# Optimization experiments

Hardware: AMD Instinct MI355X
Metric: run time of the kernel (lower is better)

## Reference

```python
import jax, jax.numpy as jnp
import numpy as np

B, T, E, H = 16, 1024, 1024, 16
DH = E // H  # 64, divisible by 4
THETA = 10000.0


def setup_inputs() -> dict:
    key = jax.random.key(0)
    ks = jax.random.split(key, 10)
    inp = {
        "hidden_states": jax.random.normal(ks[0], (B, T, E), dtype=jnp.float32),
        "rope_pos": jax.random.randint(ks[1], (B, T, 2), 0, 32, dtype=jnp.int32),
    }
    s = 0.02
    inp["Wq"] = jax.random.normal(ks[2], (E, E), dtype=jnp.float32) * s
    inp["bq"] = jnp.zeros((E,), dtype=jnp.float32)
    inp["Wk"] = jax.random.normal(ks[3], (E, E), dtype=jnp.float32) * s
    inp["bk"] = jnp.zeros((E,), dtype=jnp.float32)
    inp["Wv"] = jax.random.normal(ks[4], (E, E), dtype=jnp.float32) * s
    inp["bv"] = jnp.zeros((E,), dtype=jnp.float32)
    inp["Wo"] = jax.random.normal(ks[5], (E, E), dtype=jnp.float32) * s
    inp["bo"] = jnp.zeros((E,), dtype=jnp.float32)
    return inp


def _rotate_half(x):
    # interleaved pairs: (x0,x1,x2,x3,...) -> (-x1,x0,-x3,x2,...)
    x_even = x[..., ::2]
    x_odd = x[..., 1::2]
    return jnp.stack((-x_odd, x_even), axis=-1).reshape(x.shape)


def _apply_rope_2d(q, k, rope_pos, theta):
    Dh = q.shape[-1]
    half, quarter = Dh // 2, Dh // 4
    dtype = q.dtype
    idx = jnp.arange(quarter, dtype=dtype)
    inv = (theta ** (-2.0 * idx / quarter)).astype(dtype)  # [quarter]
    pos_h = rope_pos[..., 0].astype(dtype)[..., None]  # [B,T,1]
    pos_w = rope_pos[..., 1].astype(dtype)[..., None]
    ang_h = pos_h * inv  # [B,T,quarter]
    ang_w = pos_w * inv
    ri = lambda a: jnp.repeat(a, 2, axis=-1)[:, None]  # -> [B,1,T,half]
    cos_h, sin_h = ri(jnp.cos(ang_h)), ri(jnp.sin(ang_h))
    cos_w, sin_w = ri(jnp.cos(ang_w)), ri(jnp.sin(ang_w))
    q_h, q_w = q[..., :half], q[..., half:]
    k_h, k_w = k[..., :half], k[..., half:]
    q_h = q_h * cos_h + _rotate_half(q_h) * sin_h
    k_h = k_h * cos_h + _rotate_half(k_h) * sin_h
    q_w = q_w * cos_w + _rotate_half(q_w) * sin_w
    k_w = k_w * cos_w + _rotate_half(k_w) * sin_w
    return jnp.concatenate([q_h, q_w], axis=-1), jnp.concatenate([k_h, k_w], axis=-1)


def reference(hidden_states, rope_pos, Wq, bq, Wk, bk, Wv, bv, Wo, bo):
    b, t, e = hidden_states.shape
    scale = DH ** -0.5
    # torch nn.Linear: y = x @ W.T + b, W is [out, in]
    proj = lambda x, W, bias: jnp.einsum('bte,oe->bto', x, W) + bias
    q = proj(hidden_states, Wq, bq).reshape(b, t, H, DH).transpose(0, 2, 1, 3)
    k = proj(hidden_states, Wk, bk).reshape(b, t, H, DH).transpose(0, 2, 1, 3)
    v = proj(hidden_states, Wv, bv).reshape(b, t, H, DH).transpose(0, 2, 1, 3)
    q, k = _apply_rope_2d(q, k, rope_pos, THETA)
    # eager attention: scores in input dtype, softmax in float32
    scores = jnp.einsum('bhqd,bhkd->bhqk', q, k) * scale
    w = jax.nn.softmax(scores.astype(jnp.float32), axis=-1).astype(q.dtype)
    out = jnp.einsum('bhqk,bhkd->bhqd', w, v)
    out = out.transpose(0, 2, 1, 3).reshape(b, t, e)
    return jnp.einsum('bte,oe->bto', out, Wo) + bo
```

## Files before the change

### kernel.cpp

```cpp
#include <hip/hip_runtime.h>
#include <hip/hip_bf16.h>

#define B_  16
#define T_  1024
#define E_  1024
#define H_  16
#define DH_ 64

typedef short s16x8 __attribute__((ext_vector_type(8)));
typedef float f32x4 __attribute__((ext_vector_type(4)));
typedef unsigned short u16x4 __attribute__((ext_vector_type(4)));

__device__ __forceinline__ void async_cp16(const void* g, void* l) {
  __builtin_amdgcn_global_load_lds(
      (__attribute__((address_space(1))) unsigned int*)(g),
      (__attribute__((address_space(3))) unsigned int*)(l), 16, 0, 0);
}

__device__ __forceinline__ s16x8 frag8(const void* p) { return *(const s16x8*)p; }

__device__ __forceinline__ float fexp2(float x) {
#if __has_builtin(__builtin_amdgcn_exp2f)
  return __builtin_amdgcn_exp2f(x);
#else
  return exp2f(x);
#endif
}

__device__ __forceinline__ unsigned short f2bu(float x) {
  __hip_bfloat16 h = __float2bfloat16(x);
  return *reinterpret_cast<unsigned short*>(&h);
}

__global__ __launch_bounds__(256) void cast_f32_bf16(const float* __restrict__ in,
                                                     __hip_bfloat16* __restrict__ out,
                                                     int n4) {
  int i = blockIdx.x * 256 + threadIdx.x;
  if (i >= n4) return;
  float4 v = ((const float4*)in)[i];
  __hip_bfloat16* o = out + (size_t)i * 4;
  o[0] = __float2bfloat16(v.x);
  o[1] = __float2bfloat16(v.y);
  o[2] = __float2bfloat16(v.z);
  o[3] = __float2bfloat16(v.w);
}

#define GEMM_CORE(A_, B_PTR_, K_)                                              \
  __shared__ __align__(16) __hip_bfloat16 As[128 * 64];                        \
  __shared__ __align__(16) __hip_bfloat16 Bs[128 * 64];                        \
  const int tid  = threadIdx.x;                                                \
  const int lane = tid & 63, wave = tid >> 6;                                  \
  const int col  = lane & 15, quad = lane >> 4;                                \
  const int wm = (wave >> 1) << 6, wn = (wave & 1) << 6;                       \
  const f32x4 fzero = {0.f, 0.f, 0.f, 0.f};                                    \
  f32x4 acc[4][4];                                                             \
  _Pragma("unroll") for (int i = 0; i < 4; i++)                                \
    _Pragma("unroll") for (int j = 0; j < 4; j++) acc[i][j] = fzero;           \
  const int r8 = lane >> 3;                                                    \
  const int kgs = (lane & 7) ^ (r8 & 7);                                       \
  const char* Asrc[4]; const char* Bsrc[4]; char* Adst[4]; char* Bdst[4];      \
  _Pragma("unroll") for (int u = 0; u < 4; u++) {                              \
    int ch = u * 4 + wave;                                                     \
    int row = ch * 8 + r8;                                                     \
    Asrc[u] = (const char*)(A_ + (size_t)(bm + row) * K_) + kgs * 16;          \
    Bsrc[u] = (const char*)(B_PTR_ + (size_t)(bn + row) * K_) + kgs * 16;      \
    Adst[u] = (char*)As + ch * 1024;                                           \
    Bdst[u] = (char*)Bs + ch * 1024;                                           \
  }                                                                            \
  const int sw0 = ((quad) ^ (col & 7)) * 16;                                   \
  const int sw1 = ((quad + 4) ^ (col & 7)) * 16;                               \
  for (int kt = 0; kt < (K_ >> 6); ++kt) {                                     \
    __syncthreads();                                                           \
    const int koff = kt * 128;                                                 \
    _Pragma("unroll") for (int u = 0; u < 4; u++) {                            \
      async_cp16(Asrc[u] + koff, Adst[u]);                                     \
      async_cp16(Bsrc[u] + koff, Bdst[u]);                                     \
    }                                                                          \
    __syncthreads();                                                           \
    s16x8 af[2][4], bf[2][4];                                                  \
    _Pragma("unroll") for (int i = 0; i < 4; i++) {                            \
      af[0][i] = frag8((const char*)As + (wm + i * 16 + col) * 128 + sw0);     \
      af[1][i] = frag8((const char*)As + (wm + i * 16 + col) * 128 + sw1);     \
    }                                                                          \
    _Pragma("unroll") for (int j = 0; j < 4; j++) {                            \
      bf[0][j] = frag8((const char*)Bs + (wn + j * 16 + col) * 128 + sw0);     \
      bf[1][j] = frag8((const char*)Bs + (wn + j * 16 + col) * 128 + sw1);     \
    }                                                                          \
    _Pragma("unroll") for (int i = 0; i < 4; i++)                              \
      _Pragma("unroll") for (int j = 0; j < 4; j++) {                          \
        acc[i][j] = __builtin_amdgcn_mfma_f32_16x16x32_bf16(af[0][i], bf[0][j], acc[i][j], 0, 0, 0); \
        acc[i][j] = __builtin_amdgcn_mfma_f32_16x16x32_bf16(af[1][i], bf[1][j], acc[i][j], 0, 0, 0); \
      }                                                                        \
  }

__global__ __launch_bounds__(256, 2) void gemm_qkv(const __hip_bfloat16* __restrict__ A,
                                                   const __hip_bfloat16* __restrict__ Wqkv,
                                                   const float* __restrict__ bq,
                                                   const float* __restrict__ bk,
                                                   const float* __restrict__ bv,
                                                   __hip_bfloat16* __restrict__ Qb,
                                                   __hip_bfloat16* __restrict__ Kb,
                                                   __hip_bfloat16* __restrict__ Vt) {
  const int bm = (blockIdx.x & 127) << 7;
  const int bn = (blockIdx.x >> 7) << 7;
  GEMM_CORE(A, Wqkv, 1024)

  const int seg = bn >> 10;
  const float* bp = (seg == 0) ? bq : (seg == 1) ? bk : bv;
  float bcol[4];
#pragma unroll
  for (int j = 0; j < 4; j++) bcol[j] = bp[(bn & 1023) + wn + j * 16 + col];
#pragma unroll
  for (int i = 0; i < 4; i++) {
#pragma unroll
    for (int j = 0; j < 4; j++) {
      const int nc = (bn & 1023) + wn + j * 16 + col;
#pragma unroll
      for (int r = 0; r < 4; r++) {
        const int grow = bm + wm + i * 16 + quad * 4 + r;
        float v = acc[i][j][r] + bcol[j];
        if (seg == 0) {
          Qb[(size_t)grow * 1024 + nc] = __float2bfloat16(v);
        } else if (seg == 1) {
          Kb[(size_t)grow * 1024 + nc] = __float2bfloat16(v);
        } else {
          int bb = grow >> 10, tt = grow & 1023;
          int hh = nc >> 6, dd = nc & 63;
          Vt[(((size_t)bb * H_ + hh) * DH_ + dd) * T_ + tt] = __float2bfloat16(v);
        }
      }
    }
  }
}

__global__ __launch_bounds__(256, 2) void gemm_out(const __hip_bfloat16* __restrict__ A,
                                                   const __hip_bfloat16* __restrict__ Bw,
                                                   const float* __restrict__ bias,
                                                   float* __restrict__ Cout) {
  const int bm = (blockIdx.x & 127) << 7;
  const int bn = (blockIdx.x >> 7) << 7;
  GEMM_CORE(A, Bw, 1024)

  float bcol[4];
#pragma unroll
  for (int j = 0; j < 4; j++) bcol[j] = bias[bn + wn + j * 16 + col];
#pragma unroll
  for (int i = 0; i < 4; i++)
#pragma unroll
    for (int j = 0; j < 4; j++) {
      const int gcol = bn + wn + j * 16 + col;
#pragma unroll
      for (int r = 0; r < 4; r++) {
        const int grow = bm + wm + i * 16 + quad * 4 + r;
        Cout[(size_t)grow * 1024 + gcol] = acc[i][j][r] + bcol[j];
      }
    }
}

__global__ __launch_bounds__(256) void rope2d(__hip_bfloat16* __restrict__ Q,
                                              __hip_bfloat16* __restrict__ K,
                                              const int* __restrict__ pos) {
  const int row = blockIdx.x;
  const int t   = threadIdx.x;
  const float ph = (float)pos[row * 2 + 0];
  const float pw = (float)pos[row * 2 + 1];
  const int pd = (2 * t) & 31;
  float cs[2], sn[2];
#pragma unroll
  for (int i = 0; i < 2; i++) {
    int pdi = pd + i;
    int f = pdi & 15;
    float p = (pdi & 16) ? pw : ph;
    float inv = __expf((float)f * (-1.1512925464970229f));
    float ang = p * inv;
    cs[i] = cosf(ang);
    sn[i] = sinf(ang);
  }
  const float QSC = 0.18033688011112043f;
  size_t base = (size_t)row * E_ + 4 * t;
  {
    __hip_bfloat16* P = Q;
    float e0 = __bfloat162float(P[base + 0]);
    float e1 = __bfloat162float(P[base + 1]);
    float e2 = __bfloat162float(P[base + 2]);
    float e3 = __bfloat162float(P[base + 3]);
    P[base + 0] = __float2bfloat16((e0 * cs[0] - e1 * sn[0]) * QSC);
    P[base + 1] = __float2bfloat16((e1 * cs[0] + e0 * sn[0]) * QSC);
    P[base + 2] = __float2bfloat16((e2 * cs[1] - e3 * sn[1]) * QSC);
    P[base + 3] = __float2bfloat16((e3 * cs[1] + e2 * sn[1]) * QSC);
  }
  {
    __hip_bfloat16* P = K;
    float e0 = __bfloat162float(P[base + 0]);
    float e1 = __bfloat162float(P[base + 1]);
    float e2 = __bfloat162float(P[base + 2]);
    float e3 = __bfloat162float(P[base + 3]);
    P[base + 0] = __float2bfloat16(e0 * cs[0] - e1 * sn[0]);
    P[base + 1] = __float2bfloat16(e1 * cs[0] + e0 * sn[0]);
    P[base + 2] = __float2bfloat16(e2 * cs[1] - e3 * sn[1]);
    P[base + 3] = __float2bfloat16(e3 * cs[1] + e2 * sn[1]);
  }
}

__global__ __launch_bounds__(256, 3) void attn_flash(const __hip_bfloat16* __restrict__ Q,
                                                     const __hip_bfloat16* __restrict__ Kt,
                                                     const __hip_bfloat16* __restrict__ Vt,
                                                     __hip_bfloat16* __restrict__ Oa) {
  __shared__ __align__(16) __hip_bfloat16 QP[128 * 72];
  __shared__ __align__(16) __hip_bfloat16 Ks[64 * 72];
  __shared__ __align__(16) __hip_bfloat16 Vs[64 * 72];

  const int bid = blockIdx.x;
  const int bh = bid >> 3;
  const int b = bh >> 4, h = bh & 15;
  const int qt = bid & 7;
  const int tid = threadIdx.x;
  const int lane = tid & 63, wave = tid >> 6;
  const int col = lane & 15, quad = lane >> 4;

  const size_t qrow0 = (size_t)b * T_ + qt * 128;

#pragma unroll
  for (int cc = 0; cc < 4; ++cc) {
    int c = tid + cc * 256;
    int r = c >> 3, k8 = c & 7;
    const float4* src = (const float4*)((const char*)(Q + (qrow0 + r) * E_ + h * DH_)) + k8;
    *(float4*)((char*)QP + r * 144 + k8 * 16) = *src;
  }

  const f32x4 fzero = {0.f, 0.f, 0.f, 0.f};
  f32x4 o[2][4];
  float lr[2] = {0.f, 0.f};
#pragma unroll
  for (int g = 0; g < 2; g++)
#pragma unroll
    for (int j = 0; j < 4; j++) o[g][j] = fzero;
  s16x8 qf[2][2];
  char* Pw = (char*)QP + wave * 32 * 144;

  for (int kt2 = 0; kt2 < 16; ++kt2) {
    __syncthreads();
    const int kb = kt2 * 64;
#pragma unroll
    for (int cc = 0; cc < 4; ++cc) {
      int c = tid + cc * 256;
      if (c < 512) {
        int r = c >> 3, k8 = c & 7;
        const float4* src = (const float4*)((const char*)(Kt + ((size_t)b * T_ + kb + r) * E_ + h * DH_)) + k8;
        *(float4*)((char*)Ks + r * 144 + k8 * 16) = *src;
      } else {
        int c2 = c - 512;
        int d = c2 >> 3, k8 = c2 & 7;
        const float4* src = (const float4*)((const char*)(Vt + (((size_t)b * H_ + h) * DH_ + d) * T_ + kb)) + k8;
        *(float4*)((char*)Vs + d * 144 + k8 * 16) = *src;
      }
    }
    __syncthreads();
    if (kt2 == 0) {
#pragma unroll
      for (int g = 0; g < 2; g++) {
        qf[g][0] = frag8((const char*)QP + (g * 64 + wave * 16 + col) * 144 + quad * 16);
        qf[g][1] = frag8((const char*)QP + (g * 64 + wave * 16 + col) * 144 + 64 + quad * 16);
      }
      __syncthreads();
    }
    s16x8 kf[4][2];
#pragma unroll
    for (int ktile = 0; ktile < 4; ktile++) {
      kf[ktile][0] = frag8((const char*)Ks + (ktile * 16 + col) * 144 + quad * 16);
      kf[ktile][1] = frag8((const char*)Ks + (ktile * 16 + col) * 144 + 64 + quad * 16);
    }
#pragma unroll
    for (int g = 0; g < 2; g++) {
#pragma unroll
      for (int ktile = 0; ktile < 4; ktile++) {
        f32x4 d = fzero;
        d = __builtin_amdgcn_mfma_f32_16x16x32_bf16(kf[ktile][0], qf[g][0], d, 0, 0, 0);
        d = __builtin_amdgcn_mfma_f32_16x16x32_bf16(kf[ktile][1], qf[g][1], d, 0, 0, 0);
        float p0 = fexp2(d[0]), p1 = fexp2(d[1]), p2 = fexp2(d[2]), p3 = fexp2(d[3]);
        lr[g] += (p0 + p1) + (p2 + p3);
        u16x4 pk = {f2bu(p0), f2bu(p1), f2bu(p2), f2bu(p3)};
        *(u16x4*)(Pw + (g * 16 + col) * 144 + ktile * 32 + quad * 8) = pk;
      }
    }
    s16x8 vf[4][2];
#pragma unroll
    for (int jm = 0; jm < 4; jm++) {
      vf[jm][0] = frag8((const char*)Vs + (jm * 16 + col) * 144 + quad * 16);
      vf[jm][1] = frag8((const char*)Vs + (jm * 16 + col) * 144 + 64 + quad * 16);
    }
#pragma unroll
    for (int g = 0; g < 2; g++) {
      s16x8 pf0 = frag8(Pw + (g * 16 + col) * 144 + quad * 16);
      s16x8 pf1 = frag8(Pw + (g * 16 + col) * 144 + 64 + quad * 16);
#pragma unroll
      for (int jm = 0; jm < 4; jm++) {
        o[g][jm] = __builtin_amdgcn_mfma_f32_16x16x32_bf16(vf[jm][0], pf0, o[g][jm], 0, 0, 0);
        o[g][jm] = __builtin_amdgcn_mfma_f32_16x16x32_bf16(vf[jm][1], pf1, o[g][jm], 0, 0, 0);
      }
    }
  }
#pragma unroll
  for (int g = 0; g < 2; g++) {
    lr[g] += __shfl_xor(lr[g], 16, 64);
    lr[g] += __shfl_xor(lr[g], 32, 64);
  }
#pragma unroll
  for (int g = 0; g < 2; g++) {
    float invl = 1.f / lr[g];
    size_t grow = qrow0 + g * 64 + wave * 16 + col;
    char* obase = (char*)(Oa + grow * E_ + h * DH_);
#pragma unroll
    for (int jm = 0; jm < 4; jm++) {
      u16x4 pk = {f2bu(o[g][jm][0] * invl), f2bu(o[g][jm][1] * invl),
                  f2bu(o[g][jm][2] * invl), f2bu(o[g][jm][3] * invl)};
      *(u16x4*)(obase + jm * 32 + quad * 8) = pk;
    }
  }
}

extern "C" void kernel_launch(void* const* d_in, const int* in_sizes, int n_in,
                              void* d_out, int out_size, void* d_ws, size_t ws_size,
                              hipStream_t stream) {
  const float* X   = (const float*)d_in[0];
  const int*   pos = (const int*)d_in[1];
  const float* Wq  = (const float*)d_in[2];
  const float* bq  = (const float*)d_in[3];
  const float* Wk  = (const float*)d_in[4];
  const float* bk  = (const float*)d_in[5];
  const float* Wv  = (const float*)d_in[6];
  const float* bv  = (const float*)d_in[7];
  const float* Wo  = (const float*)d_in[8];
  const float* bo  = (const float*)d_in[9];
  float* out = (float*)d_out;

  char* ws = (char*)d_ws;
  const size_t MB = 1024 * 1024;
  __hip_bfloat16* Xb    = (__hip_bfloat16*)(ws + 0 * MB);
  __hip_bfloat16* Qb    = (__hip_bfloat16*)(ws + 32 * MB);
  __hip_bfloat16* Kb    = (__hip_bfloat16*)(ws + 64 * MB);
  __hip_bfloat16* Vtb   = (__hip_bfloat16*)(ws + 96 * MB);
  __hip_bfloat16* Wqkvb = (__hip_bfloat16*)(ws + 128 * MB);
  __hip_bfloat16* Wob   = (__hip_bfloat16*)(ws + 136 * MB);
  __hip_bfloat16* Ab    = Xb;

  cast_f32_bf16<<<16384, 256, 0, stream>>>(X,  Xb,  4194304);
  cast_f32_bf16<<<1024,  256, 0, stream>>>(Wq, Wqkvb,           262144);
  cast_f32_bf16<<<1024,  256, 0, stream>>>(Wk, Wqkvb + 1048576, 262144);
  cast_f32_bf16<<<1024,  256, 0, stream>>>(Wv, Wqkvb + 2097152, 262144);
  cast_f32_bf16<<<1024,  256, 0, stream>>>(Wo, Wob,             262144);

  gemm_qkv<<<3072, 256, 0, stream>>>(Xb, Wqkvb, bq, bk, bv, Qb, Kb, Vtb);

  rope2d<<<16384, 256, 0, stream>>>(Qb, Kb, pos);
  attn_flash<<<2048, 256, 0, stream>>>(Qb, Kb, Vtb, Ab);

  gemm_out<<<1024, 256, 0, stream>>>(Ab, Wob, bo, out);
}
```

Baseline: 445.0 us.

## Fuse 2D RoPE into QKV GEMM epilogue and batch weight casts

Moves the 2D rotary embedding and Q scaling into the QKV GEMM epilogue, using a lane shuffle to fetch each pair partner and the hardware sin/cos builtins on angles reduced to revolutions. This removes the separate rope2d kernel, which re-read and re-wrote Q and K in global memory. It also merges the four weight-cast launches into one kernel and raises the attention kernel's occupancy hint from 3 to 4 waves. The risks are extra register pressure and transcendental work in the GEMM epilogue, plus small accuracy differences from the fast sin/cos approximation.

```diff
diff --git a/kernel.cpp b/kernel.cpp
--- a/kernel.cpp
+++ b/kernel.cpp
@@ -27,6 +27,21 @@
 #endif
 }
 
+__device__ __forceinline__ float fsin2pi(float rev) {
+#if __has_builtin(__builtin_amdgcn_sinf)
+  return __builtin_amdgcn_sinf(rev);
+#else
+  return sinf(rev * 6.283185307179586f);
+#endif
+}
+__device__ __forceinline__ float fcos2pi(float rev) {
+#if __has_builtin(__builtin_amdgcn_cosf)
+  return __builtin_amdgcn_cosf(rev);
+#else
+  return cosf(rev * 6.283185307179586f);
+#endif
+}
+
 __device__ __forceinline__ unsigned short f2bu(float x) {
   __hip_bfloat16 h = __float2bfloat16(x);
   return *reinterpret_cast<unsigned short*>(&h);
@@ -37,6 +52,22 @@
                                                      int n4) {
   int i = blockIdx.x * 256 + threadIdx.x;
   if (i >= n4) return;
+  float4 v = ((const float4*)in)[i];
+  __hip_bfloat16* o = out + (size_t)i * 4;
+  o[0] = __float2bfloat16(v.x);
+  o[1] = __float2bfloat16(v.y);
+  o[2] = __float2bfloat16(v.z);
+  o[3] = __float2bfloat16(v.w);
+}
+
+__global__ __launch_bounds__(256) void cast_w4(const float* __restrict__ w0, const float* __restrict__ w1,
+                                               const float* __restrict__ w2, const float* __restrict__ w3,
+                                               __hip_bfloat16* __restrict__ o0, __hip_bfloat16* __restrict__ o1,
+                                               __hip_bfloat16* __restrict__ o2, __hip_bfloat16* __restrict__ o3) {
+  int seg = blockIdx.x >> 10;
+  const float* in = (seg == 0) ? w0 : (seg == 1) ? w1 : (seg == 2) ? w2 : w3;
+  __hip_bfloat16* out = (seg == 0) ? o0 : (seg == 1) ? o1 : (seg == 2) ? o2 : o3;
+  int i = (blockIdx.x & 1023) * 256 + threadIdx.x;
   float4 v = ((const float4*)in)[i];
   __hip_bfloat16* o = out + (size_t)i * 4;
   o[0] = __float2bfloat16(v.x);
@@ -98,6 +129,7 @@
                                                    const float* __restrict__ bq,
                                                    const float* __restrict__ bk,
                                                    const float* __restrict__ bv,
+                                                   const int* __restrict__ pos,
                                                    __hip_bfloat16* __restrict__ Qb,
                                                    __hip_bfloat16* __restrict__ Kb,
                                                    __hip_bfloat16* __restrict__ Vt) {
@@ -110,24 +142,58 @@
   float bcol[4];
 #pragma unroll
   for (int j = 0; j < 4; j++) bcol[j] = bp[(bn & 1023) + wn + j * 16 + col];
-#pragma unroll
-  for (int i = 0; i < 4; i++) {
-#pragma unroll
-    for (int j = 0; j < 4; j++) {
-      const int nc = (bn & 1023) + wn + j * 16 + col;
-#pragma unroll
-      for (int r = 0; r < 4; r++) {
-        const int grow = bm + wm + i * 16 + quad * 4 + r;
-        float v = acc[i][j][r] + bcol[j];
-        if (seg == 0) {
-          Qb[(size_t)grow * 1024 + nc] = __float2bfloat16(v);
-        } else if (seg == 1) {
-          Kb[(size_t)grow * 1024 + nc] = __float2bfloat16(v);
-        } else {
+
+  if (seg == 2) {
+#pragma unroll
+    for (int i = 0; i < 4; i++)
+#pragma unroll
+      for (int j = 0; j < 4; j++) {
+        const int nc = (bn & 1023) + wn + j * 16 + col;
+#pragma unroll
+        for (int r = 0; r < 4; r++) {
+          const int grow = bm + wm + i * 16 + quad * 4 + r;
+          float v = acc[i][j][r] + bcol[j];
           int bb = grow >> 10, tt = grow & 1023;
           int hh = nc >> 6, dd = nc & 63;
           Vt[(((size_t)bb * H_ + hh) * DH_ + dd) * T_ + tt] = __float2bfloat16(v);
         }
+      }
+    return;
+  }
+
+  const float NL2T = -1.6609640474436811f;
+  const float inv0 = fexp2(NL2T * (float)(col >> 1));
+  const float inv1 = fexp2(NL2T * (float)(8 + (col >> 1)));
+  const float sgn  = (col & 1) ? 1.f : -1.f;
+  const float R2PI = 0.15915494309189535f;
+  const float QSC  = 0.18033688011112043f;
+  const float osc  = (seg == 0) ? QSC : 1.f;
+  __hip_bfloat16* Ob = (seg == 0) ? Qb : Kb;
+  const int2* pos2 = (const int2*)pos;
+#pragma unroll
+  for (int i = 0; i < 4; i++) {
+#pragma unroll
+    for (int r = 0; r < 4; r++) {
+      const int grow = bm + wm + i * 16 + quad * 4 + r;
+      int2 pv = pos2[grow];
+      float ph = (float)pv.x, pw = (float)pv.y;
+      float cc[4], ss[4];
+#pragma unroll
+      for (int j = 0; j < 4; j++) {
+        float p   = (j < 2) ? ph : pw;
+        float inv = (j & 1) ? inv1 : inv0;
+        float rev = p * inv * R2PI;
+        rev -= floorf(rev);
+        cc[j] = fcos2pi(rev);
+        ss[j] = fsin2pi(rev);
+      }
+#pragma unroll
+      for (int j = 0; j < 4; j++) {
+        float v  = acc[i][j][r] + bcol[j];
+        float vp = __shfl_xor(v, 1, 64);
+        float rot = v * cc[j] + sgn * vp * ss[j];
+        const int nc = (bn & 1023) + wn + j * 16 + col;
+        Ob[(size_t)grow * 1024 + nc] = __float2bfloat16(rot * osc);
       }
     }
   }
@@ -157,52 +223,7 @@
     }
 }
 
-__global__ __launch_bounds__(256) void rope2d(__hip_bfloat16* __restrict__ Q,
-                                              __hip_bfloat16* __restrict__ K,
-                                              const int* __restrict__ pos) {
-  const int row = blockIdx.x;
-  const int t   = threadIdx.x;
-  const float ph = (float)pos[row * 2 + 0];
-  const float pw = (float)pos[row * 2 + 1];
-  const int pd = (2 * t) & 31;
-  float cs[2], sn[2];
-#pragma unroll
-  for (int i = 0; i < 2; i++) {
-    int pdi = pd + i;
-    int f = pdi & 15;
-    float p = (pdi & 16) ? pw : ph;
-    float inv = __expf((float)f * (-1.1512925464970229f));
-    float ang = p * inv;
-    cs[i] = cosf(ang);
-    sn[i] = sinf(ang);
-  }
-  const float QSC = 0.18033688011112043f;
-  size_t base = (size_t)row * E_ + 4 * t;
-  {
-    __hip_bfloat16* P = Q;
-    float e0 = __bfloat162float(P[base + 0]);
-    float e1 = __bfloat162float(P[base + 1]);
-    float e2 = __bfloat162float(P[base + 2]);
-    float e3 = __bfloat162float(P[base + 3]);
-    P[base + 0] = __float2bfloat16((e0 * cs[0] - e1 * sn[0]) * QSC);
-    P[base + 1] = __float2bfloat16((e1 * cs[0] + e0 * sn[0]) * QSC);
-    P[base + 2] = __float2bfloat16((e2 * cs[1] - e3 * sn[1]) * QSC);
-    P[base + 3] = __float2bfloat16((e3 * cs[1] + e2 * sn[1]) * QSC);
-  }
-  {
-    __hip_bfloat16* P = K;
-    float e0 = __bfloat162float(P[base + 0]);
-    float e1 = __bfloat162float(P[base + 1]);
-    float e2 = __bfloat162float(P[base + 2]);
-    float e3 = __bfloat162float(P[base + 3]);
-    P[base + 0] = __float2bfloat16(e0 * cs[0] - e1 * sn[0]);
-    P[base + 1] = __float2bfloat16(e1 * cs[0] + e0 * sn[0]);
-    P[base + 2] = __float2bfloat16(e2 * cs[1] - e3 * sn[1]);
-    P[base + 3] = __float2bfloat16(e3 * cs[1] + e2 * sn[1]);
-  }
-}
-
-__global__ __launch_bounds__(256, 3) void attn_flash(const __hip_bfloat16* __restrict__ Q,
+__global__ __launch_bounds__(256, 4) void attn_flash(const __hip_bfloat16* __restrict__ Q,
                                                      const __hip_bfloat16* __restrict__ Kt,
                                                      const __hip_bfloat16* __restrict__ Vt,
                                                      __hip_bfloat16* __restrict__ Oa) {
@@ -344,15 +365,12 @@
   __hip_bfloat16* Wob   = (__hip_bfloat16*)(ws + 136 * MB);
   __hip_bfloat16* Ab    = Xb;
 
-  cast_f32_bf16<<<16384, 256, 0, stream>>>(X,  Xb,  4194304);
-  cast_f32_bf16<<<1024,  256, 0, stream>>>(Wq, Wqkvb,           262144);
-  cast_f32_bf16<<<1024,  256, 0, stream>>>(Wk, Wqkvb + 1048576, 262144);
-  cast_f32_bf16<<<1024,  256, 0, stream>>>(Wv, Wqkvb + 2097152, 262144);
-  cast_f32_bf16<<<1024,  256, 0, stream>>>(Wo, Wob,             262144);
-
-  gemm_qkv<<<3072, 256, 0, stream>>>(Xb, Wqkvb, bq, bk, bv, Qb, Kb, Vtb);
-
-  rope2d<<<16384, 256, 0, stream>>>(Qb, Kb, pos);
+  cast_f32_bf16<<<16384, 256, 0, stream>>>(X, Xb, 4194304);
+  cast_w4<<<4096, 256, 0, stream>>>(Wq, Wk, Wv, Wo,
+                                    Wqkvb, Wqkvb + 1048576, Wqkvb + 2097152, Wob);
+
+  gemm_qkv<<<3072, 256, 0, stream>>>(Xb, Wqkvb, bq, bk, bv, pos, Qb, Kb, Vtb);
+
   attn_flash<<<2048, 256, 0, stream>>>(Qb, Kb, Vtb, Ab);
 
   gemm_out<<<1024, 256, 0, stream>>>(Ab, Wob, bo, out);
```

Result: slower. 501.1 us (+12.6%).
